# Optimization experiments

Hardware: AMD Instinct MI355X
Metric: run time of the kernel (lower is better)

## Reference

```python
import jax, jax.numpy as jnp
import numpy as np

LOG_2PIE = float(np.log(2 * np.pi * np.e))


def _mu_logvar(inputs, targets, W_fe, b_fe, W_lv, b_lv):
    # inputs: [Nep, N, Din], targets: [Nep, N, 1]
    phis = jax.nn.relu(jnp.einsum('end,df->enf', inputs, W_fe) + b_fe)  # [Nep, N, D]
    x = jnp.concatenate([targets, phis], axis=-1)                        # [Nep, N, D+1]
    # z = cat(mean over shots, std over shots (unbiased, as torch.std))
    z = jnp.concatenate([jnp.mean(x, axis=1), jnp.std(x, axis=1, ddof=1)], axis=-1)  # [Nep, T]
    mu = z  # use_net_for_mu=False
    logvar = jnp.clip(z @ W_lv + b_lv, -9.0, -2.0)  # Linear + Hardtanh(-9,-2)
    return mu, logvar


def _pairwise_kl(mu1, lv1, mu2, lv2):
    # KL(N(mu1_i, lv1_i) || N(mu2_j, lv2_j)) for all (i, j): [Nep, Nep]
    m1, l1 = mu1[:, None, :], lv1[:, None, :]
    m2, l2 = mu2[None, :, :], lv2[None, :, :]
    t = l2 - l1 + (jnp.exp(l1) + (m1 - m2) ** 2) * jnp.exp(-l2) - 1.0
    return 0.5 * jnp.sum(t, axis=-1)


def reference(train_inputs, train_targets, test_inputs, test_targets, W_fe, b_fe, W_lv, b_lv):
    mu_tr, lv_tr = _mu_logvar(train_inputs, train_targets, W_fe, b_fe, W_lv, b_lv)
    mu_te, lv_te = _mu_logvar(test_inputs, test_targets, W_fe, b_fe, W_lv, b_lv)
    T = mu_tr.shape[-1]
    # normal_entropy as written in source: logvar.sum() + 0.5*d*log(2*pi*e)
    H_tr = jnp.sum(lv_tr, axis=-1) + 0.5 * T * LOG_2PIE  # [Nep]
    H_te = jnp.sum(lv_te, axis=-1) + 0.5 * T * LOG_2PIE  # [Nep]
    score = (_pairwise_kl(mu_tr, lv_tr, mu_te, lv_te)
             + _pairwise_kl(mu_te, lv_te, mu_tr, lv_tr).T
             + H_tr[:, None] + H_te[None, :])
    probs = jax.nn.log_softmax(-score, axis=1)
    classes = jnp.arange(score.shape[0], dtype=jnp.int64 if jax.config.jax_enable_x64 else jnp.int32)
    return probs, classes


def setup_inputs() -> dict:
    key = jax.random.key(0)
    ks = jax.random.split(key, 6)
    Nep, N, Din, D = 256, 32, 512, 512
    T = 2 * (D + 1)
    return {
        'train_inputs': jax.random.normal(ks[0], (Nep, N, Din), jnp.float32),
        'train_targets': jax.random.normal(ks[1], (Nep, N, 1), jnp.float32),
        'test_inputs': jax.random.normal(ks[2], (Nep, N, Din), jnp.float32),
        'test_targets': jax.random.normal(ks[3], (Nep, N, 1), jnp.float32),
        'W_fe': jax.random.normal(ks[4], (Din, D), jnp.float32) / np.sqrt(Din),
        'b_fe': jnp.zeros((D,), jnp.float32),
        'W_lv': jax.random.normal(ks[5], (T, T), jnp.float32) / np.sqrt(T),
        'b_lv': jnp.zeros((T,), jnp.float32),
    }
```

## Files before the change

### kernel.cpp

```cpp
#include <hip/hip_runtime.h>
#include <math.h>

#define TDIM 1026
#define KP 1056
#define NP 1152
#define KSPLIT 7

typedef __attribute__((ext_vector_type(8))) short bf16x8;
typedef __attribute__((ext_vector_type(4))) float f32x4;

__device__ inline unsigned int pk_bf16(float a, float b) {
    unsigned int ua = __float_as_uint(a), ub = __float_as_uint(b);
    ua = (ua + 0x7FFFu + ((ua >> 16) & 1u)) >> 16;
    ub = (ub + 0x7FFFu + ((ub >> 16) & 1u)) & 0xFFFF0000u;
    return ua | ub;
}
__device__ inline unsigned short f2bf(float a) {
    unsigned int ua = __float_as_uint(a);
    return (unsigned short)((ua + 0x7FFFu + ((ua >> 16) & 1u)) >> 16);
}

__global__ __launch_bounds__(256)
void k_cvta(const float* __restrict__ tri, const float* __restrict__ tei,
            unsigned short* __restrict__ Abf)
{
    size_t g = ((size_t)blockIdx.x * 256 + threadIdx.x) * 8;
    const float* src = (g < 4194304) ? (tri + g) : (tei + (g - 4194304));
    float4 v0 = *(const float4*)(src);
    float4 v1 = *(const float4*)(src + 4);
    uint4 o;
    o.x = pk_bf16(v0.x, v0.y); o.y = pk_bf16(v0.z, v0.w);
    o.z = pk_bf16(v1.x, v1.y); o.w = pk_bf16(v1.z, v1.w);
    *(uint4*)(Abf + g) = o;
}

__global__ __launch_bounds__(256)
void k_cvtw(const float* __restrict__ W, unsigned short* __restrict__ Wt)
{
    __shared__ float T[32][33];
    const int k0 = blockIdx.y * 32, n0 = blockIdx.x * 32;
    const int t = threadIdx.x;
    {
        int ky = t >> 3, nx = (t & 7) * 4;
        float4 v = *(const float4*)(W + (size_t)(k0 + ky) * 512 + n0 + nx);
        T[nx + 0][ky] = v.x; T[nx + 1][ky] = v.y;
        T[nx + 2][ky] = v.z; T[nx + 3][ky] = v.w;
    }
    __syncthreads();
    {
        int ny = t >> 3, kx = (t & 7) * 4;
        ushort4 o;
        o.x = f2bf(T[ny][kx + 0]); o.y = f2bf(T[ny][kx + 1]);
        o.z = f2bf(T[ny][kx + 2]); o.w = f2bf(T[ny][kx + 3]);
        *(ushort4*)(Wt + (size_t)(n0 + ny) * 512 + k0 + kx) = o;
    }
}

__global__ __launch_bounds__(256)
void k_cvtwlv(const float* __restrict__ W, unsigned short* __restrict__ Wlt)
{
    __shared__ float T[32][33];
    const int n0 = blockIdx.x * 32, k0 = blockIdx.y * 32;
    const int t = threadIdx.x;
    {
        int ky = t >> 3, nx = (t & 7) * 4;
#pragma unroll
        for (int i = 0; i < 4; ++i) {
            float v = 0.f;
            if (k0 + ky < TDIM && n0 + nx + i < TDIM)
                v = W[(size_t)(k0 + ky) * TDIM + n0 + nx + i];
            T[nx + i][ky] = v;
        }
    }
    __syncthreads();
    {
        int ny = t >> 3, kx = (t & 7) * 4;
        ushort4 o;
        o.x = f2bf(T[ny][kx + 0]); o.y = f2bf(T[ny][kx + 1]);
        o.z = f2bf(T[ny][kx + 2]); o.w = f2bf(T[ny][kx + 3]);
        *(ushort4*)(Wlt + (size_t)(n0 + ny) * KP + k0 + kx) = o;
    }
}

__global__ __launch_bounds__(256)
void k_fe_mfma(const unsigned short* __restrict__ Abf,
               const unsigned short* __restrict__ Wt,
               const float* __restrict__ bfe, float* __restrict__ Z,
               unsigned short* __restrict__ Zb, float* __restrict__ muT_te)
{
    __shared__ unsigned short As[128 * 40];
    __shared__ unsigned short Bs[128 * 40];
    __shared__ float2 sbuf[4 * 128];

    const int tid  = threadIdx.x;
    const int lane = tid & 63;
    const int wave = tid >> 6;
    const int wr = wave >> 1, wc = wave & 1;
    const int m = lane & 15, quad = lane >> 4;
    const int col0 = blockIdx.x * 128;
    const int row0 = blockIdx.y * 128;

    f32x4 acc[4][4];
#pragma unroll
    for (int i = 0; i < 4; ++i)
#pragma unroll
        for (int j = 0; j < 4; ++j) acc[i][j] = (f32x4){0.f, 0.f, 0.f, 0.f};

    const int srow = tid >> 2;
    const int skc  = tid & 3;

    for (int k0 = 0; k0 < 512; k0 += 32) {
#pragma unroll
        for (int s = 0; s < 2; ++s) {
            int row = srow + s * 64;
            uint4 va = *(const uint4*)(Abf + (size_t)(row0 + row) * 512 + k0 + skc * 8);
            uint4 vb = *(const uint4*)(Wt  + (size_t)(col0 + row) * 512 + k0 + skc * 8);
            *(uint4*)(As + row * 40 + skc * 8) = va;
            *(uint4*)(Bs + row * 40 + skc * 8) = vb;
        }
        __syncthreads();
        bf16x8 af[4], bfr[4];
#pragma unroll
        for (int t2 = 0; t2 < 4; ++t2) {
            af[t2]  = *(const bf16x8*)(As + (wr * 64 + t2 * 16 + m) * 40 + quad * 8);
            bfr[t2] = *(const bf16x8*)(Bs + (wc * 64 + t2 * 16 + m) * 40 + quad * 8);
        }
#pragma unroll
        for (int ti = 0; ti < 4; ++ti)
#pragma unroll
            for (int tj = 0; tj < 4; ++tj)
                acc[ti][tj] = __builtin_amdgcn_mfma_f32_16x16x32_bf16(
                    af[ti], bfr[tj], acc[ti][tj], 0, 0, 0);
        __syncthreads();
    }

#pragma unroll
    for (int ep = 0; ep < 2; ++ep) {
#pragma unroll
        for (int tj = 0; tj < 4; ++tj) {
            int colL = wc * 64 + tj * 16 + m;
            float b = bfe[col0 + colL];
            float s1 = 0.f, s2 = 0.f;
#pragma unroll
            for (int p = 0; p < 2; ++p) {
                int ti = ep * 2 + p;
#pragma unroll
                for (int r = 0; r < 4; ++r) {
                    float v = fmaxf(acc[ti][tj][r] + b, 0.f);
                    s1 += v; s2 += v * v;
                }
            }
            s1 += __shfl_xor(s1, 16); s1 += __shfl_xor(s1, 32);
            s2 += __shfl_xor(s2, 16); s2 += __shfl_xor(s2, 32);
            if (lane < 16) sbuf[(wr * 2 + ep) * 128 + colL] = make_float2(s1, s2);
        }
    }
    __syncthreads();
    for (int idx = tid; idx < 512; idx += 256) {
        int ep = idx >> 7, cl = idx & 127;
        float2 pr = sbuf[ep * 128 + cl];
        float mean = pr.x * (1.f / 32.f);
        float var  = (pr.y - 32.f * mean * mean) * (1.f / 31.f);
        float sd   = sqrtf(fmaxf(var, 0.f));
        int e = blockIdx.y * 4 + ep;
        int f = col0 + cl;
        Z[(size_t)e * TDIM + 1 + f]   = mean;
        Z[(size_t)e * TDIM + 514 + f] = sd;
        Zb[(size_t)e * KP + 1 + f]    = f2bf(mean);
        Zb[(size_t)e * KP + 514 + f]  = f2bf(sd);
        if (e >= 256) {
            int j2 = e - 256;
            muT_te[(size_t)(1 + f) * 256 + j2]   = mean;
            muT_te[(size_t)(514 + f) * 256 + j2] = sd;
        }
    }
}

__global__ __launch_bounds__(256)
void k_tgt(const float* __restrict__ Ttr, const float* __restrict__ Tte,
           float* __restrict__ Z, unsigned short* __restrict__ Zb,
           float* __restrict__ muT_te)
{
    int e = blockIdx.x * 256 + threadIdx.x;
    if (e >= 512) return;
    const float* p = (e < 256) ? (Ttr + (size_t)e * 32) : (Tte + (size_t)(e - 256) * 32);
    float S1 = 0.f, S2 = 0.f;
#pragma unroll
    for (int n = 0; n < 32; ++n) { float v = p[n]; S1 += v; S2 += v * v; }
    float mean = S1 * (1.f / 32.f);
    float var  = (S2 - 32.f * mean * mean) * (1.f / 31.f);
    float sd   = sqrtf(fmaxf(var, 0.f));
    Z[(size_t)e * TDIM + 0]   = mean;
    Z[(size_t)e * TDIM + 513] = sd;
    Zb[(size_t)e * KP + 0]    = f2bf(mean);
    Zb[(size_t)e * KP + 513]  = f2bf(sd);
#pragma unroll
    for (int c = TDIM; c < KP; ++c) Zb[(size_t)e * KP + c] = 0;
    if (e >= 256) {
        muT_te[(size_t)0 * 256 + (e - 256)]   = mean;
        muT_te[(size_t)513 * 256 + (e - 256)] = sd;
    }
}

__global__ __launch_bounds__(256)
void k_lv_mfma(const unsigned short* __restrict__ Zb,
               const unsigned short* __restrict__ Wlt,
               float* __restrict__ Cacc)
{
    __shared__ unsigned short As[128 * 40];
    __shared__ unsigned short Bs[128 * 40];

    const int tid  = threadIdx.x;
    const int lane = tid & 63;
    const int wave = tid >> 6;
    const int wr = wave >> 1, wc = wave & 1;
    const int m = lane & 15, quad = lane >> 4;
    const int col0 = blockIdx.x * 128;
    const int row0 = blockIdx.y * 128;
    const int p    = blockIdx.z;
    const int it0  = (p < 5) ? p * 5 : 25 + (p - 5) * 4;
    const int itn  = (p < 5) ? 5 : 4;

    f32x4 acc[4][4];
#pragma unroll
    for (int i = 0; i < 4; ++i)
#pragma unroll
        for (int j = 0; j < 4; ++j) acc[i][j] = (f32x4){0.f, 0.f, 0.f, 0.f};

    const int srow = tid >> 2;
    const int skc  = tid & 3;

    for (int it = it0; it < it0 + itn; ++it) {
        int k0 = it * 32;
#pragma unroll
        for (int s = 0; s < 2; ++s) {
            int row = srow + s * 64;
            uint4 va = *(const uint4*)(Zb  + (size_t)(row0 + row) * KP + k0 + skc * 8);
            uint4 vb = *(const uint4*)(Wlt + (size_t)(col0 + row) * KP + k0 + skc * 8);
            *(uint4*)(As + row * 40 + skc * 8) = va;
            *(uint4*)(Bs + row * 40 + skc * 8) = vb;
        }
        __syncthreads();
        bf16x8 af[4], bfr[4];
#pragma unroll
        for (int t2 = 0; t2 < 4; ++t2) {
            af[t2]  = *(const bf16x8*)(As + (wr * 64 + t2 * 16 + m) * 40 + quad * 8);
            bfr[t2] = *(const bf16x8*)(Bs + (wc * 64 + t2 * 16 + m) * 40 + quad * 8);
        }
#pragma unroll
        for (int ti = 0; ti < 4; ++ti)
#pragma unroll
            for (int tj = 0; tj < 4; ++tj)
                acc[ti][tj] = __builtin_amdgcn_mfma_f32_16x16x32_bf16(
                    af[ti], bfr[tj], acc[ti][tj], 0, 0, 0);
        __syncthreads();
    }

    float* C = Cacc + (size_t)p * 512 * NP;
#pragma unroll
    for (int ti = 0; ti < 4; ++ti)
#pragma unroll
        for (int tj = 0; tj < 4; ++tj) {
            int c = col0 + wc * 64 + tj * 16 + m;
#pragma unroll
            for (int r = 0; r < 4; ++r) {
                int rg = row0 + wr * 64 + ti * 16 + quad * 4 + r;
                C[(size_t)rg * NP + c] = acc[ti][tj][r];
            }
        }
}

__global__ __launch_bounds__(256)
void k_lv_ep(const float* __restrict__ Cacc, const float* __restrict__ blv,
             float* __restrict__ E_tr, float* __restrict__ R_tr,
             float* __restrict__ E_teT, float* __restrict__ R_teT,
             float* __restrict__ Hs_te)
{
    __shared__ float Et[32][33], Rt[32][33];
    const int t = threadIdx.x;
    const int rl = t >> 3;
    const int ci = t & 7;
    const int r  = blockIdx.y * 32 + rl;
    const int c0 = blockIdx.x * 32 + ci * 4;
    const bool is_te = (blockIdx.y >= 8);

    float4 s = make_float4(0.f, 0.f, 0.f, 0.f);
#pragma unroll
    for (int p = 0; p < KSPLIT; ++p) {
        float4 v = *(const float4*)(Cacc + (size_t)p * 512 * NP + (size_t)r * NP + c0);
        s.x += v.x; s.y += v.y; s.z += v.z; s.w += v.w;
    }
    float sv[4] = {s.x, s.y, s.z, s.w};
    float lv[4], E[4], R[4];
#pragma unroll
    for (int q = 0; q < 4; ++q) {
        int c = c0 + q;
        float b = (c < TDIM) ? blv[c] : 0.f;
        float x = fminf(fmaxf(sv[q] + b, -9.f), -2.f);
        lv[q] = x; E[q] = expf(x); R[q] = expf(-x);
    }

    if (!is_te) {
        if (c0 + 1 < TDIM) {
            *(float2*)(E_tr + (size_t)r * TDIM + c0) = make_float2(E[0], E[1]);
            *(float2*)(R_tr + (size_t)r * TDIM + c0) = make_float2(R[0], R[1]);
        }
        if (c0 + 3 < TDIM) {
            *(float2*)(E_tr + (size_t)r * TDIM + c0 + 2) = make_float2(E[2], E[3]);
            *(float2*)(R_tr + (size_t)r * TDIM + c0 + 2) = make_float2(R[2], R[3]);
        }
    } else {
        float h = 0.f;
#pragma unroll
        for (int q = 0; q < 4; ++q) {
            Et[ci * 4 + q][rl] = E[q];
            Rt[ci * 4 + q][rl] = R[q];
            if (c0 + q < TDIM) h += lv[q];
        }
        h += __shfl_xor(h, 1); h += __shfl_xor(h, 2); h += __shfl_xor(h, 4);
        if (ci == 0) atomicAdd(Hs_te + (r - 256), h);
        __syncthreads();
        int cl = t >> 3, ri = (t & 7) * 4;
        int c = blockIdx.x * 32 + cl;
        if (c < TDIM) {
            int rbase = (blockIdx.y - 8) * 32 + ri;
            *(float4*)(E_teT + (size_t)c * 256 + rbase) =
                make_float4(Et[cl][ri], Et[cl][ri + 1], Et[cl][ri + 2], Et[cl][ri + 3]);
            *(float4*)(R_teT + (size_t)c * 256 + rbase) =
                make_float4(Rt[cl][ri], Rt[cl][ri + 1], Rt[cl][ri + 2], Rt[cl][ri + 3]);
        }
    }
}

__global__ __launch_bounds__(256)
void k_lv(const float* __restrict__ Z, const float* __restrict__ Wlv,
          const float* __restrict__ blv,
          float* __restrict__ E_tr, float* __restrict__ R_tr,
          float* __restrict__ E_teT, float* __restrict__ R_teT,
          float* __restrict__ Hs_te)
{
    __shared__ float Ast[16 * 68];
    __shared__ float Bs[16 * 68];
    const int tid = threadIdx.x;
    const int tx = tid & 15;
    const int ty = tid >> 4;
    const int col0 = blockIdx.x * 64;
    const int row0 = blockIdx.y * 64;

    float acc[4][4];
#pragma unroll
    for (int i = 0; i < 4; ++i)
#pragma unroll
        for (int j = 0; j < 4; ++j) acc[i][j] = 0.f;

    for (int k0 = 0; k0 < TDIM; k0 += 16) {
        {
            int row = tid >> 2, kp = tid & 3;
            const float* src = Z + (size_t)(row0 + row) * TDIM + k0 + kp * 4;
            float x0 = 0.f, x1 = 0.f, x2 = 0.f, x3 = 0.f;
            if (k0 + kp * 4 + 1 < TDIM) { float2 v = *(const float2*)(src);     x0 = v.x; x1 = v.y; }
            if (k0 + kp * 4 + 3 < TDIM) { float2 v = *(const float2*)(src + 2); x2 = v.x; x3 = v.y; }
            Ast[(kp * 4 + 0) * 68 + row] = x0;
            Ast[(kp * 4 + 1) * 68 + row] = x1;
            Ast[(kp * 4 + 2) * 68 + row] = x2;
            Ast[(kp * 4 + 3) * 68 + row] = x3;
        }
        {
            int kk = tid >> 4, cg = tid & 15;
#pragma unroll
            for (int c = 0; c < 4; ++c) {
                int col = col0 + cg * 4 + c;
                float v = 0.f;
                if (k0 + kk < TDIM && col < TDIM)
                    v = Wlv[(size_t)(k0 + kk) * TDIM + col];
                Bs[kk * 68 + cg * 4 + c] = v;
            }
        }
        __syncthreads();
#pragma unroll
        for (int kk = 0; kk < 16; ++kk) {
            float4 a = *(const float4*)(Ast + kk * 68 + ty * 4);
            float4 b = *(const float4*)(Bs + kk * 68 + tx * 4);
            float av[4] = {a.x, a.y, a.z, a.w};
            float bv[4] = {b.x, b.y, b.z, b.w};
#pragma unroll
            for (int i = 0; i < 4; ++i)
#pragma unroll
                for (int j = 0; j < 4; ++j)
                    acc[i][j] = fmaf(av[i], bv[j], acc[i][j]);
        }
        __syncthreads();
    }

    float hpart[4] = {0.f, 0.f, 0.f, 0.f};
#pragma unroll
    for (int i = 0; i < 4; ++i) {
        int r = row0 + ty * 4 + i;
#pragma unroll
        for (int j = 0; j < 4; ++j) {
            int c = col0 + tx * 4 + j;
            if (c < TDIM) {
                float lv = acc[i][j] + blv[c];
                lv = fminf(fmaxf(lv, -9.f), -2.f);
                float E = expf(lv);
                float R = expf(-lv);
                if (r < 256) {
                    E_tr[(size_t)r * TDIM + c] = E;
                    R_tr[(size_t)r * TDIM + c] = R;
                } else {
                    E_teT[(size_t)c * 256 + (r - 256)] = E;
                    R_teT[(size_t)c * 256 + (r - 256)] = R;
                    hpart[i] += lv;
                }
            }
        }
    }
    if (row0 >= 256) {
        __syncthreads();
        float* hbuf = Ast;
#pragma unroll
        for (int i = 0; i < 4; ++i) hbuf[(ty * 4 + i) * 16 + tx] = hpart[i];
        __syncthreads();
        if (tid < 64) {
            float s = 0.f;
#pragma unroll
            for (int x = 0; x < 16; ++x) s += hbuf[tid * 16 + x];
            atomicAdd(Hs_te + (row0 - 256 + tid), s);
        }
    }
}

__global__ __launch_bounds__(256)
void k_fe_f32(const float* __restrict__ Atr, const float* __restrict__ Ate,
              const float* __restrict__ Wfe, const float* __restrict__ bfe,
              float* __restrict__ Z, float* __restrict__ muT_te)
{
    __shared__ float lds[4224];
    float* Ast = lds;
    float* Bs  = lds + 2112;

    const int tid = threadIdx.x;
    const int tx = tid & 15;
    const int ty = tid >> 4;
    const int col0 = blockIdx.x * 128;
    const int row0 = blockIdx.y * 128;
    const float* A = (row0 < 8192) ? Atr : Ate;
    const int ar0 = (row0 < 8192) ? row0 : (row0 - 8192);

    float acc[8][8];
#pragma unroll
    for (int i = 0; i < 8; ++i)
#pragma unroll
        for (int j = 0; j < 8; ++j) acc[i][j] = 0.f;

    for (int k0 = 0; k0 < 512; k0 += 16) {
#pragma unroll
        for (int s = 0; s < 2; ++s) {
            int u = tid + s * 256;
            int row = u >> 2, q = u & 3;
            float4 v = *(const float4*)(A + (size_t)(ar0 + row) * 512 + k0 + q * 4);
            Ast[(q * 4 + 0) * 132 + row] = v.x;
            Ast[(q * 4 + 1) * 132 + row] = v.y;
            Ast[(q * 4 + 2) * 132 + row] = v.z;
            Ast[(q * 4 + 3) * 132 + row] = v.w;
        }
#pragma unroll
        for (int s = 0; s < 2; ++s) {
            int u = tid + s * 256;
            int kk = u >> 5, c8 = u & 31;
            float4 v = *(const float4*)(Wfe + (size_t)(k0 + kk) * 512 + col0 + c8 * 4);
            *(float4*)(Bs + kk * 132 + c8 * 4) = v;
        }
        __syncthreads();
#pragma unroll
        for (int kk = 0; kk < 16; ++kk) {
            float4 a0 = *(const float4*)(Ast + kk * 132 + ty * 8);
            float4 a1 = *(const float4*)(Ast + kk * 132 + ty * 8 + 4);
            float4 b0 = *(const float4*)(Bs + kk * 132 + tx * 4);
            float4 b1 = *(const float4*)(Bs + kk * 132 + 64 + tx * 4);
            float av[8] = {a0.x, a0.y, a0.z, a0.w, a1.x, a1.y, a1.z, a1.w};
            float bv[8] = {b0.x, b0.y, b0.z, b0.w, b1.x, b1.y, b1.z, b1.w};
#pragma unroll
            for (int i = 0; i < 8; ++i)
#pragma unroll
                for (int j = 0; j < 8; ++j)
                    acc[i][j] = fmaf(av[i], bv[j], acc[i][j]);
        }
        __syncthreads();
    }

    float2* sbuf = (float2*)lds;
#pragma unroll
    for (int j = 0; j < 8; ++j) {
        int cl = (j < 4) ? (tx * 4 + j) : (64 + tx * 4 + (j - 4));
        float b = bfe[col0 + cl];
        float s1 = 0.f, s2 = 0.f;
#pragma unroll
        for (int i = 0; i < 8; ++i) {
            float v = acc[i][j] + b;
            v = fmaxf(v, 0.f);
            s1 += v; s2 += v * v;
        }
        sbuf[ty * 128 + cl] = make_float2(s1, s2);
    }
    __syncthreads();
    for (int idx = tid; idx < 512; idx += 256) {
        int ep = idx >> 7, cl = idx & 127;
        float S1 = 0.f, S2 = 0.f;
#pragma unroll
        for (int q = 0; q < 4; ++q) {
            float2 p = sbuf[(ep * 4 + q) * 128 + cl];
            S1 += p.x; S2 += p.y;
        }
        float mean = S1 * (1.f / 32.f);
        float var  = (S2 - 32.f * mean * mean) * (1.f / 31.f);
        float sd   = sqrtf(fmaxf(var, 0.f));
        int e = (row0 >> 5) + ep;
        int f = col0 + cl;
        Z[(size_t)e * TDIM + 1 + f]   = mean;
        Z[(size_t)e * TDIM + 514 + f] = sd;
        if (e >= 256) {
            int j2 = e - 256;
            muT_te[(size_t)(1 + f) * 256 + j2]   = mean;
            muT_te[(size_t)(514 + f) * 256 + j2] = sd;
        }
    }
}

__global__ __launch_bounds__(256)
void k_tgt_f32(const float* __restrict__ Ttr, const float* __restrict__ Tte,
               float* __restrict__ Z, float* __restrict__ muT_te)
{
    int e = blockIdx.x * 256 + threadIdx.x;
    if (e >= 512) return;
    const float* p = (e < 256) ? (Ttr + (size_t)e * 32) : (Tte + (size_t)(e - 256) * 32);
    float S1 = 0.f, S2 = 0.f;
#pragma unroll
    for (int n = 0; n < 32; ++n) { float v = p[n]; S1 += v; S2 += v * v; }
    float mean = S1 * (1.f / 32.f);
    float var  = (S2 - 32.f * mean * mean) * (1.f / 31.f);
    float sd   = sqrtf(fmaxf(var, 0.f));
    Z[(size_t)e * TDIM + 0]   = mean;
    Z[(size_t)e * TDIM + 513] = sd;
    if (e >= 256) {
        muT_te[(size_t)0 * 256 + (e - 256)]   = mean;
        muT_te[(size_t)513 * 256 + (e - 256)] = sd;
    }
}

#define TCH 65
__global__ __launch_bounds__(256)
void k_pair(const float* __restrict__ Z, const float* __restrict__ E_tr,
            const float* __restrict__ R_tr, const float* __restrict__ muT_te,
            const float* __restrict__ E_teT, const float* __restrict__ R_teT,
            float* __restrict__ Sp)
{
    __shared__ float Lm[8 * 68], Le[8 * 68], Lr[8 * 68];
    const int tid = threadIdx.x;
    const int i0 = blockIdx.x * 8;
    const int t0 = blockIdx.y * TCH;
    const int tlen = min(TCH, TDIM - t0);

    if (tid < tlen) {
#pragma unroll
        for (int r = 0; r < 8; ++r) {
            size_t off = (size_t)(i0 + r) * TDIM + t0 + tid;
            Lm[r * 68 + tid] = Z[off];
            Le[r * 68 + tid] = E_tr[off];
            Lr[r * 68 + tid] = R_tr[off];
        }
    }
    __syncthreads();

    float S[8];
#pragma unroll
    for (int r = 0; r < 8; ++r) S[r] = 0.f;
    const int j = tid;
    for (int tt = 0; tt < tlen; ++tt) {
        size_t o = (size_t)(t0 + tt) * 256 + j;
        float m2 = muT_te[o], e2 = E_teT[o], r2 = R_teT[o];
#pragma unroll
        for (int r = 0; r < 8; ++r) {
            float m1 = Lm[r * 68 + tt];
            float e1 = Le[r * 68 + tt];
            float r1 = Lr[r * 68 + tt];
            float d = m1 - m2;
            S[r] += e1 * r2 + e2 * r1 + d * d * (r1 + r2);
        }
    }
#pragma unroll
    for (int r = 0; r < 8; ++r)
        Sp[((size_t)blockIdx.y * 256 + i0 + r) * 256 + j] = S[r];
}

__global__ __launch_bounds__(256)
void k_soft(const float* __restrict__ Sp, const float* __restrict__ Hs_te,
            float* __restrict__ outp)
{
    __shared__ float red[4], red2[4];
    const int i = blockIdx.x, j = threadIdx.x;
    float s = 0.f;
#pragma unroll
    for (int tc = 0; tc < 16; ++tc)
        s += Sp[((size_t)tc * 256 + i) * 256 + j];
    float v = -(0.5f * s + Hs_te[j]);

    float m = v;
#pragma unroll
    for (int o = 32; o > 0; o >>= 1) m = fmaxf(m, __shfl_xor(m, o));
    if ((j & 63) == 0) red[j >> 6] = m;
    __syncthreads();
    m = fmaxf(fmaxf(red[0], red[1]), fmaxf(red[2], red[3]));

    float p = v - m;
    float t = expf(p);
#pragma unroll
    for (int o = 32; o > 0; o >>= 1) t += __shfl_xor(t, o);
    if ((j & 63) == 0) red2[j >> 6] = t;
    __syncthreads();
    t = red2[0] + red2[1] + red2[2] + red2[3];

    outp[(size_t)i * 256 + j] = p - logf(t);
    if (i == 0) outp[65536 + j] = (float)j;
}

extern "C" void kernel_launch(void* const* d_in, const int* in_sizes, int n_in,
                              void* d_out, int out_size, void* d_ws, size_t ws_size,
                              hipStream_t stream)
{
    const float* tri = (const float*)d_in[0];
    const float* trt = (const float*)d_in[1];
    const float* tei = (const float*)d_in[2];
    const float* tet = (const float*)d_in[3];
    const float* Wfe = (const float*)d_in[4];
    const float* bfe = (const float*)d_in[5];
    const float* Wlv = (const float*)d_in[6];
    const float* blv = (const float*)d_in[7];
    float* outp = (float*)d_out;

    float* Z     = (float*)d_ws;
    float* E_tr  = Z + (size_t)512 * TDIM;
    float* R_tr  = E_tr + (size_t)256 * TDIM;
    float* muT   = R_tr + (size_t)256 * TDIM;
    float* E_teT = muT + (size_t)TDIM * 256;
    float* R_teT = E_teT + (size_t)TDIM * 256;
    float* Hs_te = R_teT + (size_t)TDIM * 256;
    float* Sp    = Hs_te + 256;
    float* endf  = Sp + (size_t)16 * 256 * 256;
    unsigned short* Abf = (unsigned short*)endf;
    unsigned short* Wt  = Abf + (size_t)16384 * 512;

    unsigned short* Wlt = (unsigned short*)Sp;
    unsigned short* Zb  = (unsigned short*)((char*)Sp + 2433024);
    float* Cacc = (float*)Abf;

    const size_t need = 11549696ull + 16777216ull + 524288ull;
    const bool fast = (ws_size >= need);

    hipMemsetAsync(Hs_te, 0, 256 * sizeof(float), stream);
    if (fast) {
        k_cvta  <<<4096, 256, 0, stream>>>(tri, tei, Abf);
        k_cvtw  <<<dim3(16, 16), 256, 0, stream>>>(Wfe, Wt);
        k_cvtwlv<<<dim3(36, 33), 256, 0, stream>>>(Wlv, Wlt);
        k_fe_mfma<<<dim3(4, 128), 256, 0, stream>>>(Abf, Wt, bfe, Z, Zb, muT);
        k_tgt   <<<2, 256, 0, stream>>>(trt, tet, Z, Zb, muT);
        k_lv_mfma<<<dim3(9, 4, KSPLIT), 256, 0, stream>>>(Zb, Wlt, Cacc);
        k_lv_ep <<<dim3(33, 16), 256, 0, stream>>>(Cacc, blv, E_tr, R_tr, E_teT, R_teT, Hs_te);
    } else {
        k_fe_f32<<<dim3(4, 128), 256, 0, stream>>>(tri, tei, Wfe, bfe, Z, muT);
        k_tgt_f32<<<2, 256, 0, stream>>>(trt, tet, Z, muT);
        k_lv    <<<dim3(17, 8), 256, 0, stream>>>(Z, Wlv, blv, E_tr, R_tr, E_teT, R_teT, Hs_te);
    }
    k_pair<<<dim3(32, 16), 256, 0, stream>>>(Z, E_tr, R_tr, muT, E_teT, R_teT, Sp);
    k_soft<<<256, 256, 0, stream>>>(Sp, Hs_te, outp);
}
```

Baseline: 170.9 us.

## Fuse fp32-to-bf16 input conversion into feature GEMM and merge weight converts

Removes the separate pass that converts the activations to bf16. The feature-extraction MFMA kernel now loads fp32 activations directly, converts them in registers, and prefetches the next K tile into registers while the current tile is computed. The two weight transpose/convert kernels are merged into one launch, and the Hs_te memset is folded into the target-stats kernel. The goal is to cut a full read/write round trip of the 16 MB activation buffer plus several launches, at the cost of reading twice as many bytes per GEMM tile and higher register pressure.

```diff
diff --git a/kernel.cpp b/kernel.cpp
--- a/kernel.cpp
+++ b/kernel.cpp
@@ -21,30 +21,27 @@
 }
 
 __global__ __launch_bounds__(256)
-void k_cvta(const float* __restrict__ tri, const float* __restrict__ tei,
-            unsigned short* __restrict__ Abf)
-{
-    size_t g = ((size_t)blockIdx.x * 256 + threadIdx.x) * 8;
-    const float* src = (g < 4194304) ? (tri + g) : (tei + (g - 4194304));
-    float4 v0 = *(const float4*)(src);
-    float4 v1 = *(const float4*)(src + 4);
-    uint4 o;
-    o.x = pk_bf16(v0.x, v0.y); o.y = pk_bf16(v0.z, v0.w);
-    o.z = pk_bf16(v1.x, v1.y); o.w = pk_bf16(v1.z, v1.w);
-    *(uint4*)(Abf + g) = o;
-}
-
-__global__ __launch_bounds__(256)
-void k_cvtw(const float* __restrict__ W, unsigned short* __restrict__ Wt)
+void k_cvtboth(const float* __restrict__ Wfe, const float* __restrict__ Wlv,
+               unsigned short* __restrict__ Wt, unsigned short* __restrict__ Wlt)
 {
     __shared__ float T[32][33];
-    const int k0 = blockIdx.y * 32, n0 = blockIdx.x * 32;
+    const int z = blockIdx.z;
+    if (z && (blockIdx.x >= 16 || blockIdx.y >= 16)) return;
+    const float* W = z ? Wfe : Wlv;
+    unsigned short* D = z ? Wt : Wlt;
+    const int S  = z ? 512 : TDIM;
+    const int DS = z ? 512 : KP;
+    const int n0 = blockIdx.x * 32, k0 = blockIdx.y * 32;
     const int t = threadIdx.x;
     {
         int ky = t >> 3, nx = (t & 7) * 4;
-        float4 v = *(const float4*)(W + (size_t)(k0 + ky) * 512 + n0 + nx);
-        T[nx + 0][ky] = v.x; T[nx + 1][ky] = v.y;
-        T[nx + 2][ky] = v.z; T[nx + 3][ky] = v.w;
+#pragma unroll
+        for (int i = 0; i < 4; ++i) {
+            float v = 0.f;
+            if (k0 + ky < S && n0 + nx + i < S)
+                v = W[(size_t)(k0 + ky) * S + n0 + nx + i];
+            T[nx + i][ky] = v;
+        }
     }
     __syncthreads();
     {
@@ -52,38 +49,12 @@
         ushort4 o;
         o.x = f2bf(T[ny][kx + 0]); o.y = f2bf(T[ny][kx + 1]);
         o.z = f2bf(T[ny][kx + 2]); o.w = f2bf(T[ny][kx + 3]);
-        *(ushort4*)(Wt + (size_t)(n0 + ny) * 512 + k0 + kx) = o;
-    }
-}
-
-__global__ __launch_bounds__(256)
-void k_cvtwlv(const float* __restrict__ W, unsigned short* __restrict__ Wlt)
-{
-    __shared__ float T[32][33];
-    const int n0 = blockIdx.x * 32, k0 = blockIdx.y * 32;
-    const int t = threadIdx.x;
-    {
-        int ky = t >> 3, nx = (t & 7) * 4;
-#pragma unroll
-        for (int i = 0; i < 4; ++i) {
-            float v = 0.f;
-            if (k0 + ky < TDIM && n0 + nx + i < TDIM)
-                v = W[(size_t)(k0 + ky) * TDIM + n0 + nx + i];
-            T[nx + i][ky] = v;
-        }
-    }
-    __syncthreads();
-    {
-        int ny = t >> 3, kx = (t & 7) * 4;
-        ushort4 o;
-        o.x = f2bf(T[ny][kx + 0]); o.y = f2bf(T[ny][kx + 1]);
-        o.z = f2bf(T[ny][kx + 2]); o.w = f2bf(T[ny][kx + 3]);
-        *(ushort4*)(Wlt + (size_t)(n0 + ny) * KP + k0 + kx) = o;
-    }
-}
-
-__global__ __launch_bounds__(256)
-void k_fe_mfma(const unsigned short* __restrict__ Abf,
+        *(ushort4*)(D + (size_t)(n0 + ny) * DS + k0 + kx) = o;
+    }
+}
+
+__global__ __launch_bounds__(256)
+void k_fe_mfma(const float* __restrict__ Atr, const float* __restrict__ Ate,
                const unsigned short* __restrict__ Wt,
                const float* __restrict__ bfe, float* __restrict__ Z,
                unsigned short* __restrict__ Zb, float* __restrict__ muT_te)
@@ -99,6 +70,8 @@
     const int m = lane & 15, quad = lane >> 4;
     const int col0 = blockIdx.x * 128;
     const int row0 = blockIdx.y * 128;
+    const float* A = (row0 < 8192) ? Atr : Ate;
+    const int ar0 = row0 & 8191;
 
     f32x4 acc[4][4];
 #pragma unroll
@@ -109,16 +82,35 @@
     const int srow = tid >> 2;
     const int skc  = tid & 3;
 
+    float4 pa0[2], pa1[2];
+    uint4  pb[2];
+
+#define FE_PRELOAD(K0)                                                              \
+    {                                                                               \
+        _Pragma("unroll")                                                           \
+        for (int s = 0; s < 2; ++s) {                                               \
+            int row = srow + s * 64;                                                \
+            const float* ap = A + (size_t)(ar0 + row) * 512 + (K0) + skc * 8;       \
+            pa0[s] = *(const float4*)(ap);                                          \
+            pa1[s] = *(const float4*)(ap + 4);                                      \
+            pb[s]  = *(const uint4*)(Wt + (size_t)(col0 + row) * 512 + (K0) + skc * 8); \
+        }                                                                           \
+    }
+
+    FE_PRELOAD(0)
     for (int k0 = 0; k0 < 512; k0 += 32) {
+        __syncthreads();
 #pragma unroll
         for (int s = 0; s < 2; ++s) {
             int row = srow + s * 64;
-            uint4 va = *(const uint4*)(Abf + (size_t)(row0 + row) * 512 + k0 + skc * 8);
-            uint4 vb = *(const uint4*)(Wt  + (size_t)(col0 + row) * 512 + k0 + skc * 8);
+            uint4 va;
+            va.x = pk_bf16(pa0[s].x, pa0[s].y); va.y = pk_bf16(pa0[s].z, pa0[s].w);
+            va.z = pk_bf16(pa1[s].x, pa1[s].y); va.w = pk_bf16(pa1[s].z, pa1[s].w);
             *(uint4*)(As + row * 40 + skc * 8) = va;
-            *(uint4*)(Bs + row * 40 + skc * 8) = vb;
-        }
-        __syncthreads();
+            *(uint4*)(Bs + row * 40 + skc * 8) = pb[s];
+        }
+        __syncthreads();
+        if (k0 + 32 < 512) FE_PRELOAD(k0 + 32)
         bf16x8 af[4], bfr[4];
 #pragma unroll
         for (int t2 = 0; t2 < 4; ++t2) {
@@ -131,7 +123,6 @@
             for (int tj = 0; tj < 4; ++tj)
                 acc[ti][tj] = __builtin_amdgcn_mfma_f32_16x16x32_bf16(
                     af[ti], bfr[tj], acc[ti][tj], 0, 0, 0);
-        __syncthreads();
     }
 
 #pragma unroll
@@ -179,8 +170,9 @@
 __global__ __launch_bounds__(256)
 void k_tgt(const float* __restrict__ Ttr, const float* __restrict__ Tte,
            float* __restrict__ Z, unsigned short* __restrict__ Zb,
-           float* __restrict__ muT_te)
-{
+           float* __restrict__ muT_te, float* __restrict__ Hs_te)
+{
+    if (blockIdx.x == 0) Hs_te[threadIdx.x] = 0.f;
     int e = blockIdx.x * 256 + threadIdx.x;
     if (e >= 512) return;
     const float* p = (e < 256) ? (Ttr + (size_t)e * 32) : (Tte + (size_t)(e - 256) * 32);
@@ -529,8 +521,10 @@
 
 __global__ __launch_bounds__(256)
 void k_tgt_f32(const float* __restrict__ Ttr, const float* __restrict__ Tte,
-               float* __restrict__ Z, float* __restrict__ muT_te)
-{
+               float* __restrict__ Z, float* __restrict__ muT_te,
+               float* __restrict__ Hs_te)
+{
+    if (blockIdx.x == 0) Hs_te[threadIdx.x] = 0.f;
     int e = blockIdx.x * 256 + threadIdx.x;
     if (e >= 512) return;
     const float* p = (e < 256) ? (Ttr + (size_t)e * 32) : (Tte + (size_t)(e - 256) * 32);
@@ -647,29 +641,25 @@
     float* Hs_te = R_teT + (size_t)TDIM * 256;
     float* Sp    = Hs_te + 256;
     float* endf  = Sp + (size_t)16 * 256 * 256;
-    unsigned short* Abf = (unsigned short*)endf;
-    unsigned short* Wt  = Abf + (size_t)16384 * 512;
 
     unsigned short* Wlt = (unsigned short*)Sp;
     unsigned short* Zb  = (unsigned short*)((char*)Sp + 2433024);
-    float* Cacc = (float*)Abf;
-
-    const size_t need = 11549696ull + 16777216ull + 524288ull;
+    float* Cacc = (float*)endf;
+    unsigned short* Wt = (unsigned short*)((char*)endf + 16515072);
+
+    const size_t need = 11549696ull + 16515072ull + 524288ull;
     const bool fast = (ws_size >= need);
 
-    hipMemsetAsync(Hs_te, 0, 256 * sizeof(float), stream);
     if (fast) {
-        k_cvta  <<<4096, 256, 0, stream>>>(tri, tei, Abf);
-        k_cvtw  <<<dim3(16, 16), 256, 0, stream>>>(Wfe, Wt);
-        k_cvtwlv<<<dim3(36, 33), 256, 0, stream>>>(Wlv, Wlt);
-        k_fe_mfma<<<dim3(4, 128), 256, 0, stream>>>(Abf, Wt, bfe, Z, Zb, muT);
-        k_tgt   <<<2, 256, 0, stream>>>(trt, tet, Z, Zb, muT);
+        k_cvtboth<<<dim3(36, 33, 2), 256, 0, stream>>>(Wfe, Wlv, Wt, Wlt);
+        k_fe_mfma<<<dim3(4, 128), 256, 0, stream>>>(tri, tei, Wt, bfe, Z, Zb, muT);
+        k_tgt    <<<2, 256, 0, stream>>>(trt, tet, Z, Zb, muT, Hs_te);
         k_lv_mfma<<<dim3(9, 4, KSPLIT), 256, 0, stream>>>(Zb, Wlt, Cacc);
-        k_lv_ep <<<dim3(33, 16), 256, 0, stream>>>(Cacc, blv, E_tr, R_tr, E_teT, R_teT, Hs_te);
+        k_lv_ep  <<<dim3(33, 16), 256, 0, stream>>>(Cacc, blv, E_tr, R_tr, E_teT, R_teT, Hs_te);
     } else {
-        k_fe_f32<<<dim3(4, 128), 256, 0, stream>>>(tri, tei, Wfe, bfe, Z, muT);
-        k_tgt_f32<<<2, 256, 0, stream>>>(trt, tet, Z, muT);
-        k_lv    <<<dim3(17, 8), 256, 0, stream>>>(Z, Wlv, blv, E_tr, R_tr, E_teT, R_teT, Hs_te);
+        k_fe_f32 <<<dim3(4, 128), 256, 0, stream>>>(tri, tei, Wfe, bfe, Z, muT);
+        k_tgt_f32<<<2, 256, 0, stream>>>(trt, tet, Z, muT, Hs_te);
+        k_lv     <<<dim3(17, 8), 256, 0, stream>>>(Z, Wlv, blv, E_tr, R_tr, E_teT, R_teT, Hs_te);
     }
     k_pair<<<dim3(32, 16), 256, 0, stream>>>(Z, E_tr, R_tr, muT, E_teT, R_teT, Sp);
     k_soft<<<256, 256, 0, stream>>>(Sp, Hs_te, outp);
```

Result: slower. 174.5 us (+2.1%).
